# Optimization experiments

Hardware: AMD Instinct MI355X
Metric: run time of the kernel (lower is better)

## Reference

```python
import jax, jax.numpy as jnp
from jax import lax
import numpy as np

NPOINT, RADIUS, NSAMPLE = 512, 0.2, 32
BN_EPS = 1e-5


def _index_points(points, idx):
    # points: [B, N, C]; idx: [B, ...] int -> [B, ..., C]
    return jax.vmap(lambda p, i: p[i])(points, idx)


def _farthest_point_sample(xyz, npoint):
    # xyz: [B, N, 3] -> [B, npoint] int32 (deterministic start at index 0)
    B, N, _ = xyz.shape
    def step(carry, _):
        distance, farthest = carry  # [B,N], [B]
        centroid = xyz[jnp.arange(B), farthest]            # [B,3]
        d = jnp.sum((xyz - centroid[:, None, :]) ** 2, -1)  # [B,N]
        distance = jnp.minimum(distance, d)
        nxt = jnp.argmax(distance, axis=-1).astype(jnp.int32)
        return (distance, nxt), farthest
    init = (jnp.full((B, N), 1e10, xyz.dtype), jnp.zeros((B,), jnp.int32))
    _, idxs = lax.scan(step, init, None, length=npoint)
    return idxs.T  # [B, npoint]


def _query_ball_point(radius, nsample, xyz, new_xyz):
    # xyz: [B,N,3], new_xyz: [B,S,3] -> [B,S,nsample] int32
    B, N, _ = xyz.shape
    S = new_xyz.shape[1]
    # squared distances [B,S,N]
    sqrdists = (jnp.sum(new_xyz ** 2, -1)[:, :, None]
                + jnp.sum(xyz ** 2, -1)[:, None, :]
                - 2.0 * jnp.einsum('bsc,bnc->bsn', new_xyz, xyz))
    group_idx = jnp.broadcast_to(jnp.arange(N, dtype=jnp.int32), (B, S, N))
    group_idx = jnp.where(sqrdists > radius * radius, N, group_idx)
    group_idx = jnp.sort(group_idx, axis=-1)[:, :, :nsample]
    first = group_idx[:, :, :1]
    return jnp.where(group_idx == N, first, group_idx)


def _mlp_layer(x, w, b, g, be):
    # x: [B, Cin, K, S]; 1x1 conv + BatchNorm2d (training stats) + relu
    y = jnp.einsum('bcks,oc->boks', x, w) + b[None, :, None, None]
    mean = jnp.mean(y, axis=(0, 2, 3), keepdims=True)
    var = jnp.mean((y - mean) ** 2, axis=(0, 2, 3), keepdims=True)
    y = (y - mean) * lax.rsqrt(var + BN_EPS)
    y = y * g[None, :, None, None] + be[None, :, None, None]
    return jax.nn.relu(y)


def setup_inputs() -> dict:
    key = jax.random.key(0)
    ks = jax.random.split(key, 16)
    inp = {
        'xyz': jax.random.uniform(ks[0], (8, 3, 16384), jnp.float32),
        'points': jax.random.normal(ks[1], (8, 3, 16384), jnp.float32),
    }
    chans = [6, 64, 64, 128]
    for i in range(3):
        cin, cout = chans[i], chans[i + 1]
        inp[f'w{i}'] = jax.random.normal(ks[2 + 4 * i], (cout, cin), jnp.float32) / np.float32(np.sqrt(cin))
        inp[f'b{i}'] = jax.random.normal(ks[3 + 4 * i], (cout,), jnp.float32) * 0.01
        inp[f'g{i}'] = jnp.ones((cout,), jnp.float32)
        inp[f'be{i}'] = jnp.zeros((cout,), jnp.float32)
    return inp


def reference(xyz, points, w0, b0, g0, be0, w1, b1, g1, be1, w2, b2, g2, be2):
    xyz_t = jnp.transpose(xyz, (0, 2, 1))      # [B,N,3]
    pts_t = jnp.transpose(points, (0, 2, 1))   # [B,N,D]
    B, N, C = xyz_t.shape

    fps_idx = _farthest_point_sample(xyz_t, NPOINT)        # [B,S]
    new_xyz = _index_points(xyz_t, fps_idx)                # [B,S,3]
    group_idx = _query_ball_point(RADIUS, NSAMPLE, xyz_t, new_xyz)  # [B,S,K]
    grouped_xyz = _index_points(xyz_t, group_idx) - new_xyz[:, :, None, :]  # [B,S,K,3]
    grouped_pts = _index_points(pts_t, group_idx)          # [B,S,K,D]
    new_points = jnp.concatenate([grouped_pts, grouped_xyz], axis=-1)  # [B,S,K,D+3]

    x = jnp.transpose(new_points, (0, 3, 2, 1))  # [B, C, K, S]
    for (w, b, g, be) in ((w0, b0, g0, be0), (w1, b1, g1, be1), (w2, b2, g2, be2)):
        x = _mlp_layer(x, w, b, g, be)
    new_feat = jnp.max(x, axis=2)                # [B, 128, S]
    new_xyz_out = jnp.transpose(new_xyz, (0, 2, 1))  # [B, 3, S]
    return (new_xyz_out, new_feat)
```

## Files before the change

### kernel.cpp

```cpp
#include <hip/hip_runtime.h>
#include <cstdint>
#include <cstddef>

#define BB 8
#define NN 16384
#define SS 512
#define KK 32

__device__ __forceinline__ float fm(float a, float b){ return __fmul_rn(a,b); }
__device__ __forceinline__ float fa(float a, float b){ return __fadd_rn(a,b); }
__device__ __forceinline__ float fsb(float a, float b){ return __fsub_rn(a,b); }

__global__ void sqnorm_kernel(const float* __restrict__ xyz, float* __restrict__ sqn){
  int gid = blockIdx.x*blockDim.x + threadIdx.x;
  int b = gid >> 14; int n = gid & (NN-1);
  const float* xb = xyz + (size_t)b*3*NN;
  float x = xb[n], y = xb[NN+n], z = xb[2*NN+n];
  sqn[gid] = fa(fa(fm(x,x),fm(y,y)),fm(z,z));
}

__global__ __launch_bounds__(1024, 4) void fps_kernel(const float* __restrict__ xyz,
                                                      float* __restrict__ nxyz,
                                                      float* __restrict__ out)
{
  int b = blockIdx.x;
  int t = threadIdx.x;
  const float* xb = xyz + (size_t)b*3*NN;
  float px[16], py[16], pz[16], dist[16];
#pragma unroll
  for (int k=0;k<16;k++){
    int n = k*1024 + t;
    px[k]=xb[n]; py[k]=xb[NN+n]; pz[k]=xb[2*NN+n];
    dist[k]=1e10f;
  }
  __shared__ unsigned long long redk[2][16];
  int wid = t >> 6, lane = t & 63;
  float cx = xb[0], cy = xb[NN], cz = xb[2*NN];
  for (int step=0; step<SS; ++step){
    if (t==0){
      float* nx = nxyz + ((size_t)b*SS + step)*3;
      nx[0]=cx; nx[1]=cy; nx[2]=cz;
      float* ox = out + (size_t)b*3*SS;
      ox[step]=cx; ox[SS+step]=cy; ox[2*SS+step]=cz;
    }
    float bv = -1.0f; int bk = 0;
#pragma unroll
    for (int k=0;k<16;k++){
      float dx=fsb(px[k],cx), dy=fsb(py[k],cy), dz=fsb(pz[k],cz);
      float d = fa(fa(fm(dx,dx),fm(dy,dy)),fm(dz,dz));
      float dk = fminf(dist[k], d);
      dist[k]=dk;
      if (dk > bv){ bv=dk; bk=k; }
    }
    int bi = (bk<<10) | t;
    unsigned long long key = ((unsigned long long)__float_as_uint(bv) << 32)
                           | (unsigned)(16384 - bi);
#pragma unroll
    for (int off=1; off<64; off<<=1){
      unsigned long long ok = __shfl_xor(key, off);
      if (ok > key) key = ok;
    }
    int par = step & 1;
    if (lane==0) redk[par][wid] = key;
    __syncthreads();
    unsigned long long k2 = redk[par][lane & 15];
#pragma unroll
    for (int off=1; off<16; off<<=1){
      unsigned long long ok = __shfl_xor(k2, off);
      if (ok > k2) k2 = ok;
    }
    int i = 16384 - (int)(unsigned)(k2 & 0xFFFFFFFFull);
    cx = xb[i]; cy = xb[NN+i]; cz = xb[2*NN+i];
  }
}

__global__ void ballq_kernel(const float* __restrict__ xyz,
                             const float* __restrict__ sqn,
                             const float* __restrict__ nxyz,
                             int* __restrict__ gidx)
{
  int wv = (blockIdx.x * (blockDim.x>>6)) + (threadIdx.x>>6);
  int lane = threadIdx.x & 63;
  int b = wv >> 9; int s = wv & (SS-1);
  const float* nx3 = nxyz + ((size_t)b*SS + s)*3;
  float nx=nx3[0], ny=nx3[1], nz=nx3[2];
  float cn = fa(fa(fm(nx,nx),fm(ny,ny)),fm(nz,nz));
  const float* xb = xyz + (size_t)b*3*NN;
  const float* sb = sqn + (size_t)b*NN;
  const float R2 = (float)(0.2*0.2);
  int* g = gidx + ((size_t)b*SS + s)*KK;
  int cnt = 0; int first_idx = 0;
  for (int base=0; base<NN; base+=64){
    int n = base + lane;
    float x=xb[n], y=xb[NN+n], z=xb[2*NN+n];
    float dot = fa(fa(fm(nx,x),fm(ny,y)),fm(nz,z));
    float sqd = fsb(fa(cn, sb[n]), fm(2.0f, dot));
    bool inb = !(sqd > R2);
    unsigned long long m = __ballot(inb);
    if (m){
      if (cnt==0) first_idx = base + __builtin_ctzll(m);
      int pre = __popcll(m & ((1ull<<lane)-1ull));
      int slot = cnt + pre;
      if (inb && slot < KK) g[slot] = n;
      cnt += __popcll(m);
      if (cnt >= KK) break;
    }
  }
  if (cnt < KK && lane >= cnt && lane < KK) g[lane] = first_idx;
}

__global__ __launch_bounds__(256) void mlp0_kernel(const float* __restrict__ xyz,
                            const float* __restrict__ pts,
                            const float* __restrict__ nxyz,
                            const int* __restrict__ gidx,
                            const float* __restrict__ w,
                            const float* __restrict__ bias,
                            float* __restrict__ y0)
{
  int gid = blockIdx.x*blockDim.x + threadIdx.x;
  int b = gid / (KK*SS);
  int r = gid % (KK*SS);
  int k = r / SS; int s = r % SS;
  int idx = gidx[((size_t)b*SS + s)*KK + k];
  const float* pb = pts + (size_t)b*3*NN;
  const float* xb = xyz + (size_t)b*3*NN;
  const float* nx3 = nxyz + ((size_t)b*SS + s)*3;
  float in[6];
  in[0]=pb[idx]; in[1]=pb[NN+idx]; in[2]=pb[2*NN+idx];
  in[3]=xb[idx]-nx3[0]; in[4]=xb[NN+idx]-nx3[1]; in[5]=xb[2*NN+idx]-nx3[2];
  float* po = y0 + (size_t)b*64*KK*SS + r;
  for (int o=0;o<64;o++){
    float acc = bias[o];
#pragma unroll
    for (int c=0;c<6;c++) acc += in[c]*w[o*6+c];
    po[(size_t)o*KK*SS] = acc;
  }
}

__global__ __launch_bounds__(256) void stats_part_kernel(const float* __restrict__ y, int C,
                                                         double* __restrict__ psum)
{
  int o = blockIdx.x >> 3; int b = blockIdx.x & 7;
  int t = threadIdx.x;
  const float4* p = (const float4*)(y + ((size_t)b*C + o)*KK*SS);
  double s1=0.0, s2=0.0;
#pragma unroll
  for (int i=0;i<16;i++){
    float4 v = p[t + i*256];
    double x0=v.x, x1=v.y, x2=v.z, x3=v.w;
    s1 += x0+x1; s1 += x2+x3;
    s2 += x0*x0 + x1*x1;
    s2 += x2*x2 + x3*x3;
  }
#pragma unroll
  for (int off=32; off>=1; off>>=1){
    s1 += __shfl_down(s1, off);
    s2 += __shfl_down(s2, off);
  }
  __shared__ double l1[4], l2[4];
  int wid = t>>6;
  if ((t&63)==0){ l1[wid]=s1; l2[wid]=s2; }
  __syncthreads();
  if (t==0){
    double t1=l1[0]+l1[1]+l1[2]+l1[3];
    double t2=l2[0]+l2[1]+l2[2]+l2[3];
    psum[(o*8+b)*2+0]=t1;
    psum[(o*8+b)*2+1]=t2;
  }
}

__global__ void stats_fin_kernel(const double* __restrict__ psum, int C,
                                 const float* __restrict__ gamma,
                                 const float* __restrict__ beta,
                                 float* __restrict__ a, float* __restrict__ c)
{
  int o = threadIdx.x;
  if (o >= C) return;
  double t1=0.0, t2=0.0;
#pragma unroll
  for (int b=0;b<8;b++){ t1 += psum[(o*8+b)*2+0]; t2 += psum[(o*8+b)*2+1]; }
  double n = (double)BB*KK*SS;
  double m = t1/n;
  double var = t2/n - m*m;
  double inv = 1.0/sqrt(var + 1e-5);
  float sc = (float)((double)gamma[o]*inv);
  a[o]=sc; c[o]=(float)((double)beta[o] - m*(double)sc);
}

template<int CIN, int COUT>
__global__ __launch_bounds__(256) void mlp_kernel(const float* __restrict__ yin,
                            const float* __restrict__ w,
                            const float* __restrict__ bias,
                            const float* __restrict__ a,
                            const float* __restrict__ cc,
                            float* __restrict__ yout)
{
  int gid = blockIdx.x*blockDim.x + threadIdx.x;
  int b = gid / (KK*SS);
  int r = gid % (KK*SS);
  const float* pin = yin + (size_t)b*CIN*KK*SS + r;
  float x[CIN];
#pragma unroll
  for (int ci=0;ci<CIN;ci++) x[ci] = fmaxf(fmaf(pin[(size_t)ci*KK*SS], a[ci], cc[ci]), 0.0f);
  float* po = yout + (size_t)b*COUT*KK*SS + r;
  for (int o=0;o<COUT;o++){
    float acc = bias[o];
#pragma unroll
    for (int ci=0;ci<CIN;ci++) acc += x[ci]*w[o*CIN+ci];
    po[(size_t)o*KK*SS] = acc;
  }
}

__global__ __launch_bounds__(256) void final_kernel(const float* __restrict__ y2,
                             const float* __restrict__ a,
                             const float* __restrict__ cc,
                             float* __restrict__ out)
{
  int gid = blockIdx.x*blockDim.x + threadIdx.x;
  int b = gid / (128*128);
  int r = gid % (128*128);
  int o = r >> 7; int s4 = (r & 127);
  const float4* p = (const float4*)(y2 + ((size_t)b*128 + o)*KK*SS) + s4;
  float sc=a[o], sh=cc[o];
  float m0=0.f,m1=0.f,m2=0.f,m3=0.f;
#pragma unroll
  for (int k=0;k<KK;k++){
    float4 v = p[k*(SS/4)];
    m0 = fmaxf(m0, fmaxf(fmaf(v.x, sc, sh), 0.0f));
    m1 = fmaxf(m1, fmaxf(fmaf(v.y, sc, sh), 0.0f));
    m2 = fmaxf(m2, fmaxf(fmaf(v.z, sc, sh), 0.0f));
    m3 = fmaxf(m3, fmaxf(fmaf(v.w, sc, sh), 0.0f));
  }
  float4* po = (float4*)(out + ((size_t)b*128 + o)*SS) + s4;
  *po = make_float4(m0,m1,m2,m3);
}

extern "C" void kernel_launch(void* const* d_in, const int* in_sizes, int n_in,
                              void* d_out, int out_size, void* d_ws, size_t ws_size,
                              hipStream_t stream)
{
  const float* xyz = (const float*)d_in[0];
  const float* pts = (const float*)d_in[1];
  const float* w0  = (const float*)d_in[2];
  const float* b0  = (const float*)d_in[3];
  const float* g0  = (const float*)d_in[4];
  const float* be0 = (const float*)d_in[5];
  const float* w1  = (const float*)d_in[6];
  const float* b1  = (const float*)d_in[7];
  const float* g1  = (const float*)d_in[8];
  const float* be1 = (const float*)d_in[9];
  const float* w2  = (const float*)d_in[10];
  const float* b2  = (const float*)d_in[11];
  const float* g2  = (const float*)d_in[12];
  const float* be2 = (const float*)d_in[13];
  float* out = (float*)d_out;

  char* ws = (char*)d_ws;
  float*  sqn  = (float*) (ws + 0);
  float*  nxyz = (float*) (ws + 524288);
  int*    gidx = (int*)   (ws + 573440);
  float*  st   = (float*) (ws + 1097728);
  double* ps0  = (double*)(ws + 1099776);
  double* ps1  = (double*)(ws + 1107968);
  double* ps2  = (double*)(ws + 1116160);
  float* a0=st,     *c0=st+64;
  float* a1=st+128, *c1=st+192;
  float* a2=st+256, *c2=st+384;
  float* y1 = (float*)(ws + 4194304);
  float* y2 = (float*)(ws + 41943040);
  float* y0 = (float*)(ws + 79691776);
  (void)ws_size; (void)in_sizes; (void)n_in; (void)out_size;

  sqnorm_kernel<<<dim3(512), dim3(256), 0, stream>>>(xyz, sqn);
  fps_kernel<<<dim3(BB), dim3(1024), 0, stream>>>(xyz, nxyz, out);
  ballq_kernel<<<dim3(1024), dim3(256), 0, stream>>>(xyz, sqn, nxyz, gidx);
  mlp0_kernel<<<dim3(512), dim3(256), 0, stream>>>(xyz, pts, nxyz, gidx, w0, b0, y0);
  stats_part_kernel<<<dim3(64*8), dim3(256), 0, stream>>>(y0, 64, ps0);
  stats_fin_kernel<<<dim3(1), dim3(64), 0, stream>>>(ps0, 64, g0, be0, a0, c0);
  mlp_kernel<64,64><<<dim3(512), dim3(256), 0, stream>>>(y0, w1, b1, a0, c0, y1);
  stats_part_kernel<<<dim3(64*8), dim3(256), 0, stream>>>(y1, 64, ps1);
  stats_fin_kernel<<<dim3(1), dim3(64), 0, stream>>>(ps1, 64, g1, be1, a1, c1);
  mlp_kernel<64,128><<<dim3(512), dim3(256), 0, stream>>>(y1, w2, b2, a1, c1, y2);
  stats_part_kernel<<<dim3(128*8), dim3(256), 0, stream>>>(y2, 128, ps2);
  stats_fin_kernel<<<dim3(1), dim3(128), 0, stream>>>(ps2, 128, g2, be2, a2, c2);
  final_kernel<<<dim3(512), dim3(256), 0, stream>>>(y2, a2, c2, out + BB*3*SS);
}
```

Measured before the change: 1.308 ms.

## Split FPS per batch across two workgroups with global-memory handshake

The farthest-point-sampling kernel now uses two 512-thread workgroups per batch, each owning half the points, instead of one 1024-thread workgroup. At every step each half reduces its local argmax and publishes it to a global slot with release semantics, then spin-waits with acquire loads for the partner's value. A small init kernel sets the slots to a sentinel first. This halves the block-level reduction width and the per-step barrier cost. In exchange it adds a cross-workgroup spin per step, which relies on both blocks being co-resident.

```diff
diff --git a/kernel.cpp b/kernel.cpp
--- a/kernel.cpp
+++ b/kernel.cpp
@@ -19,25 +19,34 @@
   sqn[gid] = fa(fa(fm(x,x),fm(y,y)),fm(z,z));
 }
 
-__global__ __launch_bounds__(1024, 4) void fps_kernel(const float* __restrict__ xyz,
-                                                      float* __restrict__ nxyz,
-                                                      float* __restrict__ out)
-{
-  int b = blockIdx.x;
+__global__ void comm_init_kernel(unsigned long long* __restrict__ comm){
+  int i = blockIdx.x*blockDim.x + threadIdx.x;
+  comm[i] = 0x8000000000000000ull;
+}
+
+__global__ __launch_bounds__(512) void fps_kernel(const float* __restrict__ xyz,
+                                                  float* __restrict__ nxyz,
+                                                  float* __restrict__ out,
+                                                  unsigned long long* __restrict__ comm)
+{
+  int bid = blockIdx.x;
+  int b = bid >> 1, half = bid & 1;
   int t = threadIdx.x;
   const float* xb = xyz + (size_t)b*3*NN;
+  const int base0 = half*8192;
   float px[16], py[16], pz[16], dist[16];
 #pragma unroll
   for (int k=0;k<16;k++){
-    int n = k*1024 + t;
+    int n = base0 + k*512 + t;
     px[k]=xb[n]; py[k]=xb[NN+n]; pz[k]=xb[2*NN+n];
     dist[k]=1e10f;
   }
-  __shared__ unsigned long long redk[2][16];
+  __shared__ unsigned long long redk[2][8];
+  __shared__ unsigned long long redp[2];
   int wid = t >> 6, lane = t & 63;
   float cx = xb[0], cy = xb[NN], cz = xb[2*NN];
   for (int step=0; step<SS; ++step){
-    if (t==0){
+    if (half==0 && t==0){
       float* nx = nxyz + ((size_t)b*SS + step)*3;
       nx[0]=cx; nx[1]=cy; nx[2]=cz;
       float* ox = out + (size_t)b*3*SS;
@@ -52,7 +61,7 @@
       dist[k]=dk;
       if (dk > bv){ bv=dk; bk=k; }
     }
-    int bi = (bk<<10) | t;
+    int bi = base0 + (bk<<9) + t;
     unsigned long long key = ((unsigned long long)__float_as_uint(bv) << 32)
                            | (unsigned)(16384 - bi);
 #pragma unroll
@@ -63,13 +72,25 @@
     int par = step & 1;
     if (lane==0) redk[par][wid] = key;
     __syncthreads();
-    unsigned long long k2 = redk[par][lane & 15];
-#pragma unroll
-    for (int off=1; off<16; off<<=1){
+    unsigned long long k2 = redk[par][lane & 7];
+#pragma unroll
+    for (int off=1; off<8; off<<=1){
       unsigned long long ok = __shfl_xor(k2, off);
       if (ok > k2) k2 = ok;
     }
-    int i = 16384 - (int)(unsigned)(k2 & 0xFFFFFFFFull);
+    unsigned long long* slot = comm + ((((size_t)b<<9) + (size_t)step)<<1);
+    if (t==0){
+      __hip_atomic_store(slot + half, k2, __ATOMIC_RELEASE, __HIP_MEMORY_SCOPE_AGENT);
+      unsigned long long kp;
+      do {
+        kp = __hip_atomic_load(slot + (half^1), __ATOMIC_ACQUIRE, __HIP_MEMORY_SCOPE_AGENT);
+      } while (kp >> 63);
+      redp[par] = kp;
+    }
+    __syncthreads();
+    unsigned long long kp = redp[par];
+    unsigned long long fin = (k2 > kp) ? k2 : kp;
+    int i = 16384 - (int)(unsigned)(fin & 0xFFFFFFFFull);
     cx = xb[i]; cy = xb[NN+i]; cz = xb[2*NN+i];
   }
 }
@@ -263,6 +284,7 @@
   double* ps0  = (double*)(ws + 1099776);
   double* ps1  = (double*)(ws + 1107968);
   double* ps2  = (double*)(ws + 1116160);
+  unsigned long long* comm = (unsigned long long*)(ws + 2097152);
   float* a0=st,     *c0=st+64;
   float* a1=st+128, *c1=st+192;
   float* a2=st+256, *c2=st+384;
@@ -272,7 +294,8 @@
   (void)ws_size; (void)in_sizes; (void)n_in; (void)out_size;
 
   sqnorm_kernel<<<dim3(512), dim3(256), 0, stream>>>(xyz, sqn);
-  fps_kernel<<<dim3(BB), dim3(1024), 0, stream>>>(xyz, nxyz, out);
+  comm_init_kernel<<<dim3(32), dim3(256), 0, stream>>>(comm);
+  fps_kernel<<<dim3(2*BB), dim3(512), 0, stream>>>(xyz, nxyz, out, comm);
   ballq_kernel<<<dim3(1024), dim3(256), 0, stream>>>(xyz, sqn, nxyz, gidx);
   mlp0_kernel<<<dim3(512), dim3(256), 0, stream>>>(xyz, pts, nxyz, gidx, w0, b0, y0);
   stats_part_kernel<<<dim3(64*8), dim3(256), 0, stream>>>(y0, 64, ps0);
```

Measured after the change: 1.413 ms. +8.0%, slower.
